# Optimization experiments

Hardware: AMD Instinct MI355X
Metric: run time of the kernel (lower is better)

Reference implementation:

```python
import jax, jax.numpy as jnp
import numpy as np

N = 8192
F0, F1, F2, F3 = 16, 64, 256, 1024
DIMS0 = (128, 128, 128)
DIMS1 = (64, 64, 64)
DIMS2 = (32, 32, 32)
DIMS3 = (16, 16, 16)
DIMS_ST1 = (16, 16, 16, 64)
DIMS_ST2 = (64, 64, 64, 64)
DIMS_TF = (4, 4, 4, 65536)
INNER = 64
OUT = 4

FACE = [(1,0,0), (-1,0,0), (0,1,0), (0,-1,0), (0,0,1), (0,0,-1)]
CORNER = [(1,1,1), (-1,-1,-1), (1,-1,-1), (-1,1,1), (1,1,-1), (-1,-1,1), (1,-1,1), (-1,1,-1)]
TEMPORAL = [1, -1]
EXP_TEMPORAL = [-64, -8, -4, -2, -1, 0, 1, 2, 4, 8, 64]
FACE_OFF = np.asarray(FACE, np.int32)                                    # [6,3]
BASIC_ST = np.asarray([s + (tt,) for s in FACE + CORNER for tt in TEMPORAL], np.int32)  # [28,4]
EXP_ST = np.asarray([s + (tt,) for s in CORNER for tt in EXP_TEMPORAL], np.int32)       # [88,4]

TOTAL_FEAT = 7 * (F0 + F1 + F2 + F3) + BASIC_ST.shape[0] * 64 + BASIC_ST.shape[0] * 8 + EXP_ST.shape[0] * 8  # 12240


def scale_idx(x, dims):
    # torch: (x * (dims - 1)).long()  -- truncation; x in [0,1) so same as floor
    return (x * (jnp.asarray(dims, x.dtype) - 1)).astype(jnp.int32)


def gather(table, idx):
    if idx.shape[-1] == 3:
        return table[idx[..., 0], idx[..., 1], idx[..., 2]]
    return table[idx[..., 0], idx[..., 1], idx[..., 2], idx[..., 3]]


def lookup_neighbors(table, dims, base_idx, offsets):
    # base_idx: [N,D] int; offsets: [K,D] int -> [N, K*F]
    nidx = (base_idx[:, None, :] + jnp.asarray(offsets, jnp.int32)) % jnp.asarray(dims, jnp.int32)
    f = gather(table, nidx)  # [N,K,F]
    return f.reshape(f.shape[0], -1)


def rmsnorm(x, scale, eps=1e-8):
    norm = jnp.sqrt(jnp.sum(x * x, axis=-1, keepdims=True))
    rms = norm * (x.shape[-1] ** -0.5)
    return scale * (x / (rms + eps))


def setup_inputs() -> dict:
    key = jax.random.key(0)
    ks = jax.random.split(key, 16)
    inp = {
        "pos": jax.random.uniform(ks[0], (N, 3), jnp.float32),
        "dir": jax.random.normal(ks[1], (N, 3), jnp.float32),
        "t": jax.random.uniform(ks[2], (N,), jnp.float32),
        "table0": jax.random.normal(ks[3], DIMS0 + (F0,), jnp.float32),
        "table1": jax.random.normal(ks[4], DIMS1 + (F1,), jnp.float32),
        "table2": jax.random.normal(ks[5], DIMS2 + (F2,), jnp.float32),
        "table3": jax.random.normal(ks[6], DIMS3 + (F3,), jnp.float32),
        "st1": jax.random.normal(ks[7], DIMS_ST1 + (64,), jnp.float32),
        "st2": jax.random.normal(ks[8], DIMS_ST2 + (8,), jnp.float32),
        "tf3": jax.random.normal(ks[9], DIMS_TF + (8,), jnp.float32),
        "rms_scale": jnp.ones((TOTAL_FEAT,), jnp.float32),
        "w_down": jax.random.normal(ks[10], (TOTAL_FEAT, INNER), jnp.float32) * 0.02,
        "w_final": jax.random.normal(ks[11], (INNER + 3 + 1, OUT), jnp.float32) * 0.1,
        "b_final": jnp.zeros((OUT,), jnp.float32),
    }
    return inp


def reference(pos, dir, t, table0, table1, table2, table3, st1, st2, tf3,
              rms_scale, w_down, w_final, b_final):
    idx0 = scale_idx(pos, DIMS0)
    idx1 = scale_idx(pos, DIMS1)
    idx2 = scale_idx(pos, DIMS2)
    idx3 = scale_idx(pos, DIMS3)
    # original quirk: t.unsqueeze(-1) [N,1] broadcasts against 4-d dims -> [N,4]
    t_idx = scale_idx(t[:, None], DIMS_ST1)

    f0 = jnp.concatenate([gather(table0, idx0), lookup_neighbors(table0, DIMS0, idx0, FACE_OFF)], -1)
    f1 = jnp.concatenate([gather(table1, idx1), lookup_neighbors(table1, DIMS1, idx1, FACE_OFF)], -1)
    f2 = jnp.concatenate([gather(table2, idx2), lookup_neighbors(table2, DIMS2, idx2, FACE_OFF)], -1)
    f3 = jnp.concatenate([gather(table3, idx3), lookup_neighbors(table3, DIMS3, idx3, FACE_OFF)], -1)

    st_f1 = lookup_neighbors(st1, DIMS_ST1, t_idx, BASIC_ST)
    st_f2 = lookup_neighbors(st2, DIMS_ST2, t_idx, BASIC_ST)
    tf = lookup_neighbors(tf3, DIMS_TF, t_idx, EXP_ST)

    all_f = jax.nn.relu(jnp.concatenate([f0, f1, f2, f3, st_f1, st_f2, tf], -1))  # [N, TOTAL_FEAT]
    h = jax.nn.relu(rmsnorm(all_f, rms_scale) @ w_down)                          # [N, INNER]
    final_in = jnp.concatenate([h, dir, t[:, None]], -1)                          # [N, INNER+4]
    return jax.nn.sigmoid(final_in @ w_final + b_final)                           # [N, OUT]
```

## Files before the change

kernel.cpp:

```cpp
#include <hip/hip_runtime.h>
#include <math.h>

#define TOTF   12240
#define NU     3060
#define KTILE  256
#define NTILES 48
#define ASTRIDE 264
#define MQ     16
#define NTHR   512

typedef float f32x4  __attribute__((ext_vector_type(4)));
typedef short bf16x8 __attribute__((ext_vector_type(8)));

__constant__ int OFF7[7][3] = {
    {0,0,0},{1,0,0},{-1,0,0},{0,1,0},{0,-1,0},{0,0,1},{0,0,-1}
};
__constant__ int SPAT14[14][3] = {
    {1,0,0},{-1,0,0},{0,1,0},{0,-1,0},{0,0,1},{0,0,-1},
    {1,1,1},{-1,-1,-1},{1,-1,-1},{-1,1,1},{1,1,-1},{-1,-1,1},{1,-1,1},{-1,1,-1}
};
__constant__ int CORN8[8][3] = {
    {1,1,1},{-1,-1,-1},{1,-1,-1},{-1,1,1},{1,1,-1},{-1,-1,1},{1,-1,1},{-1,1,-1}
};
__constant__ int EXPT[11] = {-64,-8,-4,-2,-1,0,1,2,4,8,64};

static __device__ __forceinline__ unsigned short f2bf(float f) {
    unsigned int u = __float_as_uint(f);
    u += 0x7fffu + ((u >> 16) & 1u);
    return (unsigned short)(u >> 16);
}

__global__ __launch_bounds__(256)
void wconv_kernel(const float* __restrict__ w, const float* __restrict__ s,
                  unsigned short* __restrict__ Wt) {
    int id = blockIdx.x * 256 + threadIdx.x;
    if (id < TOTF * 64) {
        int k = id >> 6, j = id & 63;
        Wt[j * TOTF + k] = f2bf(w[id] * s[k]);
    }
}

__global__ __launch_bounds__(NTHR)
void st_fused_kernel(const float* __restrict__ pos, const float* __restrict__ dirv,
                     const float* __restrict__ t,
                     const float* __restrict__ tb0, const float* __restrict__ tb1,
                     const float* __restrict__ tb2, const float* __restrict__ tb3,
                     const float* __restrict__ st1, const float* __restrict__ st2,
                     const float* __restrict__ tf3,
                     const unsigned short* __restrict__ Wt,
                     const float* __restrict__ w_final, const float* __restrict__ b_final,
                     float* __restrict__ out, int N)
{
    __shared__ unsigned long long bases_s[172 * MQ];
    __shared__ __align__(16) unsigned short Atile[MQ * ASTRIDE];
    __shared__ __align__(16) unsigned short Wtile[64 * ASTRIDE];
    __shared__ float ssq_s[MQ];
    __shared__ float inv_s[MQ];

    const int tid = threadIdx.x;
    const int q0  = blockIdx.x * MQ;
    const int q   = tid & 15;
    const int qg  = min(q0 + q, N - 1);

    {
        const float px = pos[qg*3+0], py = pos[qg*3+1], pz = pos[qg*3+2];
        const float tv = t[qg];
        const int b0x=(int)(px*127.f), b0y=(int)(py*127.f), b0z=(int)(pz*127.f);
        const int b1x=(int)(px*63.f),  b1y=(int)(py*63.f),  b1z=(int)(pz*63.f);
        const int b2x=(int)(px*31.f),  b2y=(int)(py*31.f),  b2z=(int)(pz*31.f);
        const int b3x=(int)(px*15.f),  b3y=(int)(py*15.f),  b3z=(int)(pz*15.f);
        const int i15=(int)(tv*15.f),  i63=(int)(tv*63.f);

        for (int ent = tid >> 4; ent < 172; ent += 32) {
            unsigned long long a;
            if (ent < 7) {
                int ix=(b0x+OFF7[ent][0]+128)&127, iy=(b0y+OFF7[ent][1]+128)&127, iz=(b0z+OFF7[ent][2]+128)&127;
                a = (unsigned long long)tb0 + (unsigned long long)((ix*128+iy)*128+iz) * 64ull;
            } else if (ent < 14) {
                int l=ent-7;
                int ix=(b1x+OFF7[l][0]+64)&63, iy=(b1y+OFF7[l][1]+64)&63, iz=(b1z+OFF7[l][2]+64)&63;
                a = (unsigned long long)tb1 + (unsigned long long)((ix*64+iy)*64+iz) * 256ull;
            } else if (ent < 21) {
                int l=ent-14;
                int ix=(b2x+OFF7[l][0]+32)&31, iy=(b2y+OFF7[l][1]+32)&31, iz=(b2z+OFF7[l][2]+32)&31;
                a = (unsigned long long)tb2 + (unsigned long long)((ix*32+iy)*32+iz) * 1024ull;
            } else if (ent < 28) {
                int l=ent-21;
                int ix=(b3x+OFF7[l][0]+16)&15, iy=(b3y+OFF7[l][1]+16)&15, iz=(b3z+OFF7[l][2]+16)&15;
                a = (unsigned long long)tb3 + (unsigned long long)((ix*16+iy)*16+iz) * 4096ull;
            } else if (ent < 56) {
                int r=ent-28, s=r>>1, tt=(r&1)?-1:1;
                int ix=(i15+SPAT14[s][0]+16)&15, iy=(i15+SPAT14[s][1]+16)&15, iz=(i15+SPAT14[s][2]+16)&15;
                int it=(i63+tt+64)&63;
                a = (unsigned long long)st1 + (unsigned long long)(((ix*16+iy)*16+iz)*64+it) * 256ull;
            } else if (ent < 84) {
                int r=ent-56, s=r>>1, tt=(r&1)?-1:1;
                int ix=(i15+SPAT14[s][0]+64)&63, iy=(i15+SPAT14[s][1]+64)&63, iz=(i15+SPAT14[s][2]+64)&63;
                int it=(i63+tt+64)&63;
                a = (unsigned long long)st2 + (unsigned long long)(((ix*64+iy)*64+iz)*64+it) * 32ull;
            } else {
                int r=ent-84, c=r/11, ti=r-c*11;
                int ix=(i15+CORN8[c][0]+4)&3, iy=(i15+CORN8[c][1]+4)&3, iz=(i15+CORN8[c][2]+4)&3;
                int it=(i63+EXPT[ti]+65536)&65535;
                a = (unsigned long long)tf3 + (unsigned long long)(((ix*4+iy)*4+iz)*65536+it) * 32ull;
            }
            bases_s[ent * MQ + q] = a;
        }
    }
    if (tid < MQ) ssq_s[tid] = 0.f;

    const int lane = tid & 63, w = tid >> 6;
    const int jt = w & 3, ksp = w >> 2;
    const int mrow = lane & 15, kq = (lane >> 4) * 8;
    f32x4 acc = {0.f, 0.f, 0.f, 0.f};
    float ss = 0.f;

    for (int tile = 0; tile < NTILES; ++tile) {
        __syncthreads();
        const int u0 = tile * 64;
        #pragma unroll
        for (int it2 = 0; it2 < 2; ++it2) {
            const int e = ((it2 * NTHR) + tid) >> 4;
            const int u = u0 + e;
            float4 v = make_float4(0.f, 0.f, 0.f, 0.f);
            if (u < NU) {
                int ent, f;
                if (u < 28)        { ent = u >> 2;                 f = u & 3; }
                else if (u < 140)  { int x=u-28;   ent=7 +(x>>4);  f = x & 15; }
                else if (u < 588)  { int x=u-140;  ent=14+(x>>6);  f = x & 63; }
                else if (u < 2380) { int x=u-588;  ent=21+(x>>8);  f = x & 255; }
                else if (u < 2828) { int x=u-2380; ent=28+(x>>4);  f = x & 15; }
                else if (u < 2884) { int x=u-2828; ent=56+(x>>1);  f = x & 1; }
                else               { int x=u-2884; ent=84+(x>>1);  f = x & 1; }
                unsigned long long a = bases_s[ent * MQ + q] + (unsigned long long)(f * 16);
                v = *(const float4*)(uintptr_t)a;
            }
            float r0 = fmaxf(v.x, 0.f), r1 = fmaxf(v.y, 0.f);
            float r2 = fmaxf(v.z, 0.f), r3 = fmaxf(v.w, 0.f);
            ss += r0*r0 + r1*r1 + r2*r2 + r3*r3;
            ushort4 pk;
            pk.x = f2bf(r0); pk.y = f2bf(r1); pk.z = f2bf(r2); pk.w = f2bf(r3);
            *(ushort4*)&Atile[q * ASTRIDE + e * 4] = pk;
        }
        const int k0 = tile * KTILE;
        #pragma unroll
        for (int it2 = 0; it2 < 4; ++it2) {
            const int idx = it2 * NTHR + tid;
            const int j = idx >> 5, c = idx & 31;
            const int kg = k0 + c * 8;
            uint4 val = make_uint4(0u, 0u, 0u, 0u);
            if (kg < TOTF) val = *(const uint4*)(Wt + j * TOTF + kg);
            *(uint4*)&Wtile[j * ASTRIDE + c * 8] = val;
        }
        __syncthreads();
        #pragma unroll
        for (int s2 = 0; s2 < 4; ++s2) {
            const int kk = (ksp * 4 + s2) * 32 + kq;
            bf16x8 av = *(const bf16x8*)&Atile[mrow * ASTRIDE + kk];
            bf16x8 bv = *(const bf16x8*)&Wtile[(jt * 16 + mrow) * ASTRIDE + kk];
            acc = __builtin_amdgcn_mfma_f32_16x16x32_bf16(av, bv, acc, 0, 0, 0);
        }
    }

    __syncthreads();
    atomicAdd(&ssq_s[q], ss);
    float* h_s = (float*)Atile;
    if (ksp == 0) {
        #pragma unroll
        for (int r = 0; r < 4; ++r)
            h_s[((lane >> 4) * 4 + r) * 64 + jt * 16 + (lane & 15)] = acc[r];
    }
    __syncthreads();
    if (ksp == 1) {
        #pragma unroll
        for (int r = 0; r < 4; ++r)
            h_s[((lane >> 4) * 4 + r) * 64 + jt * 16 + (lane & 15)] += acc[r];
    }
    __syncthreads();
    if (tid < MQ) {
        const float RSQ = 9.0395480320866816e-03f;
        inv_s[tid] = 1.0f / (sqrtf(ssq_s[tid]) * RSQ + 1e-8f);
    }
    __syncthreads();
    if (tid < 64) {
        const int qq = tid >> 2, o = tid & 3;
        const int qqg = q0 + qq;
        if (qqg < N) {
            const float inv = inv_s[qq];
            float s = b_final[o];
            float hs = 0.f;
            #pragma unroll 8
            for (int j = 0; j < 64; ++j)
                hs += fmaxf(h_s[qq * 64 + j], 0.f) * w_final[j * 4 + o];
            s += hs * inv;
            s += dirv[qqg*3+0] * w_final[64*4 + o];
            s += dirv[qqg*3+1] * w_final[65*4 + o];
            s += dirv[qqg*3+2] * w_final[66*4 + o];
            s += t[qqg]        * w_final[67*4 + o];
            out[qqg * 4 + o] = 1.0f / (1.0f + expf(-s));
        }
    }
}

extern "C" void kernel_launch(void* const* d_in, const int* in_sizes, int n_in,
                              void* d_out, int out_size, void* d_ws, size_t ws_size,
                              hipStream_t stream) {
    const float* pos  = (const float*)d_in[0];
    const float* dirv = (const float*)d_in[1];
    const float* t    = (const float*)d_in[2];
    const float* tb0  = (const float*)d_in[3];
    const float* tb1  = (const float*)d_in[4];
    const float* tb2  = (const float*)d_in[5];
    const float* tb3  = (const float*)d_in[6];
    const float* st1  = (const float*)d_in[7];
    const float* st2  = (const float*)d_in[8];
    const float* tf3  = (const float*)d_in[9];
    const float* rs   = (const float*)d_in[10];
    const float* wd   = (const float*)d_in[11];
    const float* wf   = (const float*)d_in[12];
    const float* bf   = (const float*)d_in[13];
    float* out = (float*)d_out;
    unsigned short* Wt = (unsigned short*)d_ws;

    const int N = in_sizes[2];
    wconv_kernel<<<dim3((TOTF * 64 + 255) / 256), dim3(256), 0, stream>>>(wd, rs, Wt);
    st_fused_kernel<<<dim3((N + MQ - 1) / MQ), dim3(NTHR), 0, stream>>>(
        pos, dirv, t, tb0, tb1, tb2, tb3, st1, st2, tf3, Wt, wf, bf, out, N);
}
```

Measured before the change: 890.2 us.

## Double-buffer gather and weight tiles with register prefetch, one barrier per tile

Restructures the K loop into a software pipeline. Global loads for the next tile (gathered features and weights) go into registers while MFMAs run on the current LDS buffer, and are written to the alternate buffer afterwards. This leaves one barrier per tile instead of two. The K tile is halved to fit two buffers in LDS, and per-entry 64-bit base pointers are replaced by 32-bit offsets to save shared memory. The out-of-range weight index is clamped rather than zero-filled, which relies on the A tile being zero in that region. The cost is more loop iterations, each with less work.

```diff
diff --git a/kernel.cpp b/kernel.cpp
--- a/kernel.cpp
+++ b/kernel.cpp
@@ -3,9 +3,9 @@
 
 #define TOTF   12240
 #define NU     3060
-#define KTILE  256
-#define NTILES 48
-#define ASTRIDE 264
+#define KTILE  128
+#define NTILES 96
+#define ASTRIDE 136
 #define MQ     16
 #define NTHR   512
 
@@ -51,15 +51,16 @@
                      const float* __restrict__ w_final, const float* __restrict__ b_final,
                      float* __restrict__ out, int N)
 {
-    __shared__ unsigned long long bases_s[172 * MQ];
-    __shared__ __align__(16) unsigned short Atile[MQ * ASTRIDE];
-    __shared__ __align__(16) unsigned short Wtile[64 * ASTRIDE];
+    __shared__ unsigned int offs_s[172 * MQ];
+    __shared__ __align__(16) unsigned short Atile[2][MQ * ASTRIDE];
+    __shared__ __align__(16) unsigned short Wtile[2][64 * ASTRIDE];
     __shared__ float ssq_s[MQ];
     __shared__ float inv_s[MQ];
 
     const int tid = threadIdx.x;
     const int q0  = blockIdx.x * MQ;
     const int q   = tid & 15;
+    const int e   = tid >> 4;
     const int qg  = min(q0 + q, N - 1);
 
     {
@@ -72,94 +73,101 @@
         const int i15=(int)(tv*15.f),  i63=(int)(tv*63.f);
 
         for (int ent = tid >> 4; ent < 172; ent += 32) {
-            unsigned long long a;
+            unsigned off;
             if (ent < 7) {
                 int ix=(b0x+OFF7[ent][0]+128)&127, iy=(b0y+OFF7[ent][1]+128)&127, iz=(b0z+OFF7[ent][2]+128)&127;
-                a = (unsigned long long)tb0 + (unsigned long long)((ix*128+iy)*128+iz) * 64ull;
+                off = (unsigned)(((ix*128+iy)*128+iz) * 64);
             } else if (ent < 14) {
                 int l=ent-7;
                 int ix=(b1x+OFF7[l][0]+64)&63, iy=(b1y+OFF7[l][1]+64)&63, iz=(b1z+OFF7[l][2]+64)&63;
-                a = (unsigned long long)tb1 + (unsigned long long)((ix*64+iy)*64+iz) * 256ull;
+                off = (unsigned)(((ix*64+iy)*64+iz) * 256);
             } else if (ent < 21) {
                 int l=ent-14;
                 int ix=(b2x+OFF7[l][0]+32)&31, iy=(b2y+OFF7[l][1]+32)&31, iz=(b2z+OFF7[l][2]+32)&31;
-                a = (unsigned long long)tb2 + (unsigned long long)((ix*32+iy)*32+iz) * 1024ull;
+                off = (unsigned)(((ix*32+iy)*32+iz) * 1024);
             } else if (ent < 28) {
                 int l=ent-21;
                 int ix=(b3x+OFF7[l][0]+16)&15, iy=(b3y+OFF7[l][1]+16)&15, iz=(b3z+OFF7[l][2]+16)&15;
-                a = (unsigned long long)tb3 + (unsigned long long)((ix*16+iy)*16+iz) * 4096ull;
+                off = (unsigned)(((ix*16+iy)*16+iz) * 4096);
             } else if (ent < 56) {
                 int r=ent-28, s=r>>1, tt=(r&1)?-1:1;
                 int ix=(i15+SPAT14[s][0]+16)&15, iy=(i15+SPAT14[s][1]+16)&15, iz=(i15+SPAT14[s][2]+16)&15;
                 int it=(i63+tt+64)&63;
-                a = (unsigned long long)st1 + (unsigned long long)(((ix*16+iy)*16+iz)*64+it) * 256ull;
+                off = (unsigned)((((ix*16+iy)*16+iz)*64+it) * 256);
             } else if (ent < 84) {
                 int r=ent-56, s=r>>1, tt=(r&1)?-1:1;
                 int ix=(i15+SPAT14[s][0]+64)&63, iy=(i15+SPAT14[s][1]+64)&63, iz=(i15+SPAT14[s][2]+64)&63;
                 int it=(i63+tt+64)&63;
-                a = (unsigned long long)st2 + (unsigned long long)(((ix*64+iy)*64+iz)*64+it) * 32ull;
+                off = (unsigned)((((ix*64+iy)*64+iz)*64+it) * 32);
             } else {
                 int r=ent-84, c=r/11, ti=r-c*11;
                 int ix=(i15+CORN8[c][0]+4)&3, iy=(i15+CORN8[c][1]+4)&3, iz=(i15+CORN8[c][2]+4)&3;
                 int it=(i63+EXPT[ti]+65536)&65535;
-                a = (unsigned long long)tf3 + (unsigned long long)(((ix*4+iy)*4+iz)*65536+it) * 32ull;
+                off = (unsigned)((((ix*4+iy)*4+iz)*65536+it) * 32);
             }
-            bases_s[ent * MQ + q] = a;
+            offs_s[ent * MQ + q] = off;
         }
     }
     if (tid < MQ) ssq_s[tid] = 0.f;
+    __syncthreads();
 
     const int lane = tid & 63, w = tid >> 6;
     const int jt = w & 3, ksp = w >> 2;
     const int mrow = lane & 15, kq = (lane >> 4) * 8;
+    const int wj = tid >> 4;
+    const int wc = tid & 15;
     f32x4 acc = {0.f, 0.f, 0.f, 0.f};
     float ss = 0.f;
 
+    float4 av; uint4 wva, wvb;
+
+    auto LOADS = [&](int tt) {
+        const int u = tt * 32 + e;
+        av = make_float4(0.f, 0.f, 0.f, 0.f);
+        if (u < NU) {
+            unsigned long long a;
+            if (u < 28)        { a = (unsigned long long)tb0 + offs_s[(u >> 2) * MQ + q]          + (unsigned)((u & 3)   * 16); }
+            else if (u < 140)  { int x = u - 28;   a = (unsigned long long)tb1 + offs_s[(7  + (x >> 4)) * MQ + q] + (unsigned)((x & 15)  * 16); }
+            else if (u < 588)  { int x = u - 140;  a = (unsigned long long)tb2 + offs_s[(14 + (x >> 6)) * MQ + q] + (unsigned)((x & 63)  * 16); }
+            else if (u < 2380) { int x = u - 588;  a = (unsigned long long)tb3 + offs_s[(21 + (x >> 8)) * MQ + q] + (unsigned)((x & 255) * 16); }
+            else if (u < 2828) { int x = u - 2380; a = (unsigned long long)st1 + offs_s[(28 + (x >> 4)) * MQ + q] + (unsigned)((x & 15)  * 16); }
+            else if (u < 2884) { int x = u - 2828; a = (unsigned long long)st2 + offs_s[(56 + (x >> 1)) * MQ + q] + (unsigned)((x & 1)   * 16); }
+            else               { int x = u - 2884; a = (unsigned long long)tf3 + offs_s[(84 + (x >> 1)) * MQ + q] + (unsigned)((x & 1)   * 16); }
+            av = *(const float4*)(uintptr_t)a;
+        }
+        const int kg = min(tt * KTILE + wc * 8, TOTF - 8);
+        wva = *(const uint4*)(Wt + wj * TOTF + kg);
+        wvb = *(const uint4*)(Wt + (wj + 32) * TOTF + kg);
+    };
+
+    auto PWRITE = [&](int b) {
+        float r0 = fmaxf(av.x, 0.f), r1 = fmaxf(av.y, 0.f);
+        float r2 = fmaxf(av.z, 0.f), r3 = fmaxf(av.w, 0.f);
+        ss += r0*r0 + r1*r1 + r2*r2 + r3*r3;
+        ushort4 pk;
+        pk.x = f2bf(r0); pk.y = f2bf(r1); pk.z = f2bf(r2); pk.w = f2bf(r3);
+        *(ushort4*)&Atile[b][q * ASTRIDE + e * 4] = pk;
+        *(uint4*)&Wtile[b][wj * ASTRIDE + wc * 8] = wva;
+        *(uint4*)&Wtile[b][(wj + 32) * ASTRIDE + wc * 8] = wvb;
+    };
+
+    LOADS(0);
+    PWRITE(0);
+
     for (int tile = 0; tile < NTILES; ++tile) {
+        const int cur = tile & 1;
         __syncthreads();
-        const int u0 = tile * 64;
+        if (tile + 1 < NTILES) LOADS(tile + 1);
+        const unsigned short* At = Atile[cur];
+        const unsigned short* Bt = Wtile[cur];
         #pragma unroll
-        for (int it2 = 0; it2 < 2; ++it2) {
-            const int e = ((it2 * NTHR) + tid) >> 4;
-            const int u = u0 + e;
-            float4 v = make_float4(0.f, 0.f, 0.f, 0.f);
-            if (u < NU) {
-                int ent, f;
-                if (u < 28)        { ent = u >> 2;                 f = u & 3; }
-                else if (u < 140)  { int x=u-28;   ent=7 +(x>>4);  f = x & 15; }
-                else if (u < 588)  { int x=u-140;  ent=14+(x>>6);  f = x & 63; }
-                else if (u < 2380) { int x=u-588;  ent=21+(x>>8);  f = x & 255; }
-                else if (u < 2828) { int x=u-2380; ent=28+(x>>4);  f = x & 15; }
-                else if (u < 2884) { int x=u-2828; ent=56+(x>>1);  f = x & 1; }
-                else               { int x=u-2884; ent=84+(x>>1);  f = x & 1; }
-                unsigned long long a = bases_s[ent * MQ + q] + (unsigned long long)(f * 16);
-                v = *(const float4*)(uintptr_t)a;
-            }
-            float r0 = fmaxf(v.x, 0.f), r1 = fmaxf(v.y, 0.f);
-            float r2 = fmaxf(v.z, 0.f), r3 = fmaxf(v.w, 0.f);
-            ss += r0*r0 + r1*r1 + r2*r2 + r3*r3;
-            ushort4 pk;
-            pk.x = f2bf(r0); pk.y = f2bf(r1); pk.z = f2bf(r2); pk.w = f2bf(r3);
-            *(ushort4*)&Atile[q * ASTRIDE + e * 4] = pk;
-        }
-        const int k0 = tile * KTILE;
-        #pragma unroll
-        for (int it2 = 0; it2 < 4; ++it2) {
-            const int idx = it2 * NTHR + tid;
-            const int j = idx >> 5, c = idx & 31;
-            const int kg = k0 + c * 8;
-            uint4 val = make_uint4(0u, 0u, 0u, 0u);
-            if (kg < TOTF) val = *(const uint4*)(Wt + j * TOTF + kg);
-            *(uint4*)&Wtile[j * ASTRIDE + c * 8] = val;
-        }
-        __syncthreads();
-        #pragma unroll
-        for (int s2 = 0; s2 < 4; ++s2) {
-            const int kk = (ksp * 4 + s2) * 32 + kq;
-            bf16x8 av = *(const bf16x8*)&Atile[mrow * ASTRIDE + kk];
-            bf16x8 bv = *(const bf16x8*)&Wtile[(jt * 16 + mrow) * ASTRIDE + kk];
-            acc = __builtin_amdgcn_mfma_f32_16x16x32_bf16(av, bv, acc, 0, 0, 0);
-        }
+        for (int s2 = 0; s2 < 2; ++s2) {
+            const int kk = ksp * 64 + s2 * 32 + kq;
+            bf16x8 avf = *(const bf16x8*)&At[mrow * ASTRIDE + kk];
+            bf16x8 bvf = *(const bf16x8*)&Bt[(jt * 16 + mrow) * ASTRIDE + kk];
+            acc = __builtin_amdgcn_mfma_f32_16x16x32_bf16(avf, bvf, acc, 0, 0, 0);
+        }
+        if (tile + 1 < NTILES) PWRITE(cur ^ 1);
     }
 
     __syncthreads();
```

Measured after the change: 875.4 us. About the same (-1.7%).
